# Optimization experiments

Hardware: AMD Instinct MI355X
Metric: run time of the kernel (lower is better)

## Reference

```python
import jax, jax.numpy as jnp
import numpy as np

NUM_HEADS = 32
HEAD_DIM = 128
HEAVY_BUDGET = 256
RECENT_BUDGET = 256
ROPE_BASE = 10000.0


def _rope_tables(position_ids, head_dim, dtype):
    inv_freq = 1.0 / (ROPE_BASE ** (jnp.arange(0, head_dim, 2, dtype=jnp.float32) / head_dim))
    freqs = position_ids.astype(jnp.float32)[..., None] * inv_freq  # [b, s, hd/2]
    emb = jnp.concatenate([freqs, freqs], axis=-1)                  # [b, s, hd]
    return jnp.cos(emb).astype(dtype), jnp.sin(emb).astype(dtype)


def _rotate_half(x):
    h = x.shape[-1] // 2
    return jnp.concatenate([-x[..., h:], x[..., :h]], axis=-1)


def setup_inputs() -> dict:
    key = jax.random.key(0)
    k1, k2, k3, k4, k5 = jax.random.split(key, 5)
    b, s, d = 1, 2048, 4096
    hidden_states = jax.random.normal(k1, (b, s, d), dtype=jnp.float32)
    # additive causal mask, as HF passes into forward
    neg = jnp.finfo(jnp.float32).min
    causal = jnp.tril(jnp.ones((s, s), dtype=bool))
    attention_mask = jnp.where(causal, 0.0, neg).astype(jnp.float32)[None, None]  # [1,1,s,s]
    position_ids = jnp.arange(s, dtype=jnp.int32)[None]  # [1, s]
    scale = 0.02
    Wq = jax.random.normal(k2, (d, d), dtype=jnp.float32) * scale
    Wk = jax.random.normal(k3, (d, d), dtype=jnp.float32) * scale
    Wv = jax.random.normal(k4, (d, d), dtype=jnp.float32) * scale
    Wo = jax.random.normal(k5, (d, d), dtype=jnp.float32) * scale
    return {"hidden_states": hidden_states, "attention_mask": attention_mask,
            "position_ids": position_ids, "Wq": Wq, "Wk": Wk, "Wv": Wv, "Wo": Wo}


def reference(hidden_states, attention_mask, position_ids, Wq, Wk, Wv, Wo):
    b, s, d = hidden_states.shape
    H, hd = NUM_HEADS, HEAD_DIM
    kv = s  # prefill: no past_key_value, masks reset

    # projections: nn.Linear(x) = x @ W.T
    q = (hidden_states @ Wq.T).reshape(b, s, H, hd).transpose(0, 2, 1, 3)  # [b,H,s,hd]
    k = (hidden_states @ Wk.T).reshape(b, s, H, hd).transpose(0, 2, 1, 3)
    v = (hidden_states @ Wv.T).reshape(b, s, H, hd).transpose(0, 2, 1, 3)

    cos, sin = _rope_tables(position_ids, hd, q.dtype)  # [b,s,hd]
    cos, sin = cos[:, None], sin[:, None]               # broadcast over heads
    q = q * cos + _rotate_half(q) * sin
    k = k * cos + _rotate_half(k) * sin

    attn = jnp.einsum('bhqd,bhkd->bhqk', q, k) / np.float32(np.sqrt(hd))
    neg = jnp.finfo(attn.dtype).min
    attn = jnp.maximum(attn + attention_mask, neg)
    # attention_masks_next is None on the first (prefill) call -> no multiplicative mask here
    attn = jax.nn.softmax(attn.astype(jnp.float32), axis=-1).astype(q.dtype)  # [b,H,s,kv]

    # running per-head score accumulation: sum over batch and query dims
    scores = attn.sum(axis=0).sum(axis=1)  # [H, kv]; previous_scores is None at prefill

    # heavy-hitter eviction mask for the next decode step (kv+1 columns)
    mask = jnp.ones((H, kv + 1), dtype=attn.dtype)
    # attn_tokens_all (=kv) > cache_budget, recent_budget > 0:
    mask = mask.at[:, :kv + 1 - RECENT_BUDGET].set(0.0)
    selected = scores[:, :kv - RECENT_BUDGET]                    # drop recent region
    _, keep_topk = jax.lax.top_k(selected, HEAVY_BUDGET)         # [H, heavy]
    mask = mask.at[jnp.arange(H)[:, None], keep_topk].set(1.0)   # scatter heavy hitters
    # torch aliasing: score_mask = attn_mask[:, :-1]; score_mask[:, -recent:] = 1 mutates attn_mask too
    mask = mask.at[:, kv - RECENT_BUDGET:kv].set(1.0)
    attention_masks_next = mask[None, :, None, :]                # [1,H,1,kv+1]
    previous_scores = scores * mask[:, :kv]                      # masked score state

    out = jnp.einsum('bhqk,bhkd->bhqd', attn, v)                 # [b,H,s,hd]
    out = out.transpose(0, 2, 1, 3).reshape(b, s, d) @ Wo.T
    return out, attention_masks_next, previous_scores
```

## Files before the change

kernel.cpp:

```cpp
#include <hip/hip_runtime.h>
#include <hip/hip_bf16.h>
#include <cmath>

#define S_LEN 2048
#define DMODEL 4096
#define NH 32
#define HDIM 128
#define HEAVY 256
#define RECENT 256
#define ATTN_SCALE 0.08838834764831845f
#define NEGBIG -3.0e38f
#define MB (1024ull * 1024ull)

typedef __attribute__((ext_vector_type(8))) short short8v;
typedef __attribute__((ext_vector_type(4))) short short4v;
typedef __attribute__((ext_vector_type(4))) float floatx4;

__device__ inline ushort f2bf(float x) {
  __hip_bfloat16 h = __float2bfloat16(x);
  return __builtin_bit_cast(ushort, h);
}
struct Split3 {
  short a, b, c;
};
__device__ inline Split3 split3(float x) {
  unsigned u = __float_as_uint(x);
  unsigned u1 = u & 0xFFFF0000u;
  float r1 = x - __uint_as_float(u1);
  unsigned u2 = __float_as_uint(r1) & 0xFFFF0000u;
  float r2 = r1 - __uint_as_float(u2);
  unsigned u3 = __float_as_uint(r2);
  Split3 o;
  o.a = (short)(u1 >> 16);
  o.b = (short)(u2 >> 16);
  o.c = (short)(u3 >> 16);
  return o;
}

__device__ __forceinline__ void gl_lds16(const short* gsrc, short* ldst) {
  __builtin_amdgcn_global_load_lds((const __attribute__((address_space(1))) void*)gsrc,
                                   (__attribute__((address_space(3))) void*)ldst, 16, 0, 0);
}

__global__ void split_mat(const float* __restrict__ X, short* __restrict__ Xa,
                          short* __restrict__ Xb, short* __restrict__ Xc, int n4) {
  int stride = gridDim.x * blockDim.x;
  for (int i = blockIdx.x * blockDim.x + threadIdx.x; i < n4; i += stride) {
    float4 v = reinterpret_cast<const float4*>(X)[i];
    float vv[4] = {v.x, v.y, v.z, v.w};
    short4v a, b, c;
#pragma unroll
    for (int j = 0; j < 4; j++) {
      Split3 t = split3(vv[j]);
      a[j] = t.a; b[j] = t.b; c[j] = t.c;
    }
    reinterpret_cast<short4v*>(Xa)[i] = a;
    reinterpret_cast<short4v*>(Xb)[i] = b;
    reinterpret_cast<short4v*>(Xc)[i] = c;
  }
}

__global__ __launch_bounds__(256) void norms_kernel(const float* __restrict__ Qf,
                                                    const float* __restrict__ Kf,
                                                    float* __restrict__ qn,
                                                    float* __restrict__ mk2p) {
  const int h = blockIdx.x >> 4, ch = blockIdx.x & 15;
  const int wv = threadIdx.x >> 6, lane = threadIdx.x & 63;
  __shared__ float wmax[4];
  float mx = 0.f;
  for (int i = 0; i < 32; i++) {
    int r = ch * 128 + wv * 32 + i;
    const float2 qv =
        *reinterpret_cast<const float2*>(&Qf[(size_t)r * DMODEL + h * HDIM + lane * 2]);
    const float2 kv =
        *reinterpret_cast<const float2*>(&Kf[(size_t)r * DMODEL + h * HDIM + lane * 2]);
    float sq = qv.x * qv.x + qv.y * qv.y;
    float sk = kv.x * kv.x + kv.y * kv.y;
#pragma unroll
    for (int off = 1; off <= 32; off <<= 1) {
      sq += __shfl_xor(sq, off);
      sk += __shfl_xor(sk, off);
    }
    if (lane == 0) qn[h * S_LEN + r] = sqrtf(sq);
    mx = fmaxf(mx, sk);
  }
  if (lane == 0) wmax[wv] = mx;
  __syncthreads();
  if (threadIdx.x == 0)
    mk2p[blockIdx.x] = fmaxf(fmaxf(wmax[0], wmax[1]), fmaxf(wmax[2], wmax[3]));
}

__global__ __launch_bounds__(256) void gemm6p(
    const short* __restrict__ Aag, const short* __restrict__ Abg, const short* __restrict__ Acg,
    const short* __restrict__ Bag, const short* __restrict__ Bbg, const short* __restrict__ Bcg,
    float* __restrict__ C, int M, int N, int K) {
  __shared__ short Aa[128 * 40], Ab[128 * 40], Ac[128 * 40];
  __shared__ short Ba[128 * 40], Bb[128 * 40], Bc[128 * 40];
  const int tid = threadIdx.x;
  const int w = tid >> 6, l = tid & 63, g = l >> 4, ln = l & 15;
  const int wm = w >> 1, wn = w & 1;
  const int row0 = blockIdx.y * 128, col0 = blockIdx.x * 128;
  floatx4 acc[4][4] = {};
  for (int k0 = 0; k0 < K; k0 += 32) {
    __syncthreads();
#pragma unroll
    for (int i = 0; i < 2; i++) {
      int id = tid + i * 256;
      int r = id >> 2, c = id & 3;
      size_t ga = (size_t)(row0 + r) * K + k0 + c * 8;
      size_t gb = (size_t)(col0 + r) * K + k0 + c * 8;
      int o = r * 40 + c * 8;
      *reinterpret_cast<short8v*>(&Aa[o]) = *reinterpret_cast<const short8v*>(&Aag[ga]);
      *reinterpret_cast<short8v*>(&Ab[o]) = *reinterpret_cast<const short8v*>(&Abg[ga]);
      *reinterpret_cast<short8v*>(&Ac[o]) = *reinterpret_cast<const short8v*>(&Acg[ga]);
      *reinterpret_cast<short8v*>(&Ba[o]) = *reinterpret_cast<const short8v*>(&Bag[gb]);
      *reinterpret_cast<short8v*>(&Bb[o]) = *reinterpret_cast<const short8v*>(&Bbg[gb]);
      *reinterpret_cast<short8v*>(&Bc[o]) = *reinterpret_cast<const short8v*>(&Bcg[gb]);
    }
    __syncthreads();
#pragma unroll
    for (int i = 0; i < 4; i++) {
      int ar = (wm * 64 + i * 16 + ln) * 40 + g * 8;
      short8v a1 = *reinterpret_cast<const short8v*>(&Aa[ar]);
      short8v a2 = *reinterpret_cast<const short8v*>(&Ab[ar]);
      short8v a3 = *reinterpret_cast<const short8v*>(&Ac[ar]);
#pragma unroll
      for (int j = 0; j < 4; j++) {
        int br = (wn * 64 + j * 16 + ln) * 40 + g * 8;
        short8v b1 = *reinterpret_cast<const short8v*>(&Ba[br]);
        short8v b2 = *reinterpret_cast<const short8v*>(&Bb[br]);
        short8v b3 = *reinterpret_cast<const short8v*>(&Bc[br]);
        acc[i][j] = __builtin_amdgcn_mfma_f32_16x16x32_bf16(a1, b1, acc[i][j], 0, 0, 0);
        acc[i][j] = __builtin_amdgcn_mfma_f32_16x16x32_bf16(a1, b2, acc[i][j], 0, 0, 0);
        acc[i][j] = __builtin_amdgcn_mfma_f32_16x16x32_bf16(a2, b1, acc[i][j], 0, 0, 0);
        acc[i][j] = __builtin_amdgcn_mfma_f32_16x16x32_bf16(a1, b3, acc[i][j], 0, 0, 0);
        acc[i][j] = __builtin_amdgcn_mfma_f32_16x16x32_bf16(a2, b2, acc[i][j], 0, 0, 0);
        acc[i][j] = __builtin_amdgcn_mfma_f32_16x16x32_bf16(a3, b1, acc[i][j], 0, 0, 0);
      }
    }
  }
#pragma unroll
  for (int i = 0; i < 4; i++)
#pragma unroll
    for (int j = 0; j < 4; j++)
#pragma unroll
      for (int r = 0; r < 4; r++)
        C[(size_t)(row0 + wm * 64 + i * 16 + g * 4 + r) * N + col0 + wn * 64 + j * 16 + ln] =
            acc[i][j][r];
}

__global__ __launch_bounds__(256) void gemm6h(const short* __restrict__ Aag,
                                              const short* __restrict__ Abg,
                                              const short* __restrict__ Acg,
                                              const float* __restrict__ B,
                                              float* __restrict__ C, int M, int N, int K) {
  __shared__ short Aa[128 * 40], Ab[128 * 40], Ac[128 * 40];
  __shared__ short Ba[128 * 40], Bb[128 * 40], Bc[128 * 40];
  const int tid = threadIdx.x;
  const int w = tid >> 6, l = tid & 63, g = l >> 4, ln = l & 15;
  const int wm = w >> 1, wn = w & 1;
  const int row0 = blockIdx.y * 128, col0 = blockIdx.x * 128;
  floatx4 acc[4][4] = {};
  for (int k0 = 0; k0 < K; k0 += 32) {
    __syncthreads();
#pragma unroll
    for (int i = 0; i < 2; i++) {
      int id = tid + i * 256;
      int r = id >> 2, c = id & 3;
      size_t ga = (size_t)(row0 + r) * K + k0 + c * 8;
      int o = r * 40 + c * 8;
      *reinterpret_cast<short8v*>(&Aa[o]) = *reinterpret_cast<const short8v*>(&Aag[ga]);
      *reinterpret_cast<short8v*>(&Ab[o]) = *reinterpret_cast<const short8v*>(&Abg[ga]);
      *reinterpret_cast<short8v*>(&Ac[o]) = *reinterpret_cast<const short8v*>(&Acg[ga]);
    }
#pragma unroll
    for (int i = 0; i < 4; i++) {
      int id = tid + i * 256;
      int r = id >> 3, c4 = id & 7;
      float4 bv = *reinterpret_cast<const float4*>(&B[(size_t)(col0 + r) * K + k0 + c4 * 4]);
      float bf[4] = {bv.x, bv.y, bv.z, bv.w};
      short4v b1, b2, b3;
#pragma unroll
      for (int j = 0; j < 4; j++) {
        Split3 t = split3(bf[j]);
        b1[j] = t.a; b2[j] = t.b; b3[j] = t.c;
      }
      int o = r * 40 + c4 * 4;
      *reinterpret_cast<short4v*>(&Ba[o]) = b1;
      *reinterpret_cast<short4v*>(&Bb[o]) = b2;
      *reinterpret_cast<short4v*>(&Bc[o]) = b3;
    }
    __syncthreads();
#pragma unroll
    for (int i = 0; i < 4; i++) {
      int ar = (wm * 64 + i * 16 + ln) * 40 + g * 8;
      short8v a1 = *reinterpret_cast<const short8v*>(&Aa[ar]);
      short8v a2 = *reinterpret_cast<const short8v*>(&Ab[ar]);
      short8v a3 = *reinterpret_cast<const short8v*>(&Ac[ar]);
#pragma unroll
      for (int j = 0; j < 4; j++) {
        int br = (wn * 64 + j * 16 + ln) * 40 + g * 8;
        short8v b1 = *reinterpret_cast<const short8v*>(&Ba[br]);
        short8v b2 = *reinterpret_cast<const short8v*>(&Bb[br]);
        short8v b3 = *reinterpret_cast<const short8v*>(&Bc[br]);
        acc[i][j] = __builtin_amdgcn_mfma_f32_16x16x32_bf16(a1, b1, acc[i][j], 0, 0, 0);
        acc[i][j] = __builtin_amdgcn_mfma_f32_16x16x32_bf16(a1, b2, acc[i][j], 0, 0, 0);
        acc[i][j] = __builtin_amdgcn_mfma_f32_16x16x32_bf16(a2, b1, acc[i][j], 0, 0, 0);
        acc[i][j] = __builtin_amdgcn_mfma_f32_16x16x32_bf16(a1, b3, acc[i][j], 0, 0, 0);
        acc[i][j] = __builtin_amdgcn_mfma_f32_16x16x32_bf16(a2, b2, acc[i][j], 0, 0, 0);
        acc[i][j] = __builtin_amdgcn_mfma_f32_16x16x32_bf16(a3, b1, acc[i][j], 0, 0, 0);
      }
    }
  }
#pragma unroll
  for (int i = 0; i < 4; i++)
#pragma unroll
    for (int j = 0; j < 4; j++)
#pragma unroll
      for (int r = 0; r < 4; r++)
        C[(size_t)(row0 + wm * 64 + i * 16 + g * 4 + r) * N + col0 + wn * 64 + j * 16 + ln] =
            acc[i][j][r];
}

__global__ __launch_bounds__(256) void gemm_bf1(const float* __restrict__ A,
                                                const float* __restrict__ B,
                                                float* __restrict__ C, int M, int N, int K) {
  __shared__ short Ah[128 * 40];
  __shared__ short Bh[128 * 40];
  const int tid = threadIdx.x;
  const int w = tid >> 6, l = tid & 63, g = l >> 4, ln = l & 15;
  const int wm = w >> 1, wn = w & 1;
  const int row0 = blockIdx.y * 128, col0 = blockIdx.x * 128;
  floatx4 acc[4][4] = {};
  for (int k0 = 0; k0 < K; k0 += 32) {
    __syncthreads();
#pragma unroll
    for (int i = 0; i < 4; i++) {
      int id = tid + i * 256;
      int r = id >> 3, c4 = id & 7;
      float4 av = *reinterpret_cast<const float4*>(&A[(size_t)(row0 + r) * K + k0 + c4 * 4]);
      float4 bv = *reinterpret_cast<const float4*>(&B[(size_t)(col0 + r) * K + k0 + c4 * 4]);
      short4v ah, bh;
      ah[0] = (short)f2bf(av.x); ah[1] = (short)f2bf(av.y);
      ah[2] = (short)f2bf(av.z); ah[3] = (short)f2bf(av.w);
      bh[0] = (short)f2bf(bv.x); bh[1] = (short)f2bf(bv.y);
      bh[2] = (short)f2bf(bv.z); bh[3] = (short)f2bf(bv.w);
      *reinterpret_cast<short4v*>(&Ah[r * 40 + c4 * 4]) = ah;
      *reinterpret_cast<short4v*>(&Bh[r * 40 + c4 * 4]) = bh;
    }
    __syncthreads();
#pragma unroll
    for (int i = 0; i < 4; i++) {
      short8v a = *reinterpret_cast<const short8v*>(&Ah[(wm * 64 + i * 16 + ln) * 40 + g * 8]);
#pragma unroll
      for (int j = 0; j < 4; j++) {
        short8v b = *reinterpret_cast<const short8v*>(&Bh[(wn * 64 + j * 16 + ln) * 40 + g * 8]);
        acc[i][j] = __builtin_amdgcn_mfma_f32_16x16x32_bf16(a, b, acc[i][j], 0, 0, 0);
      }
    }
  }
#pragma unroll
  for (int i = 0; i < 4; i++)
#pragma unroll
    for (int j = 0; j < 4; j++)
#pragma unroll
      for (int r = 0; r < 4; r++)
        C[(size_t)(row0 + wm * 64 + i * 16 + g * 4 + r) * N + col0 + wn * 64 + j * 16 + ln] =
            acc[i][j][r];
}

__global__ __launch_bounds__(256) void gemm_vbt(const short* __restrict__ Ab2,
                                                const float* __restrict__ B,
                                                ushort* __restrict__ Vt, int M, int N, int K) {
  __shared__ short Ah[128 * 40];
  __shared__ short Bh[128 * 40];
  const int tid = threadIdx.x;
  const int w = tid >> 6, l = tid & 63, g = l >> 4, ln = l & 15;
  const int wm = w >> 1, wn = w & 1;
  const int row0 = blockIdx.y * 128, col0 = blockIdx.x * 128;
  floatx4 acc[4][4] = {};
  for (int k0 = 0; k0 < K; k0 += 32) {
    __syncthreads();
#pragma unroll
    for (int i = 0; i < 2; i++) {
      int id = tid + i * 256;
      int r = id >> 2, c = id & 3;
      *reinterpret_cast<short8v*>(&Ah[r * 40 + c * 8]) =
          *reinterpret_cast<const short8v*>(&Ab2[(size_t)(row0 + r) * K + k0 + c * 8]);
    }
#pragma unroll
    for (int i = 0; i < 4; i++) {
      int id = tid + i * 256;
      int r = id >> 3, c4 = id & 7;
      float4 bv = *reinterpret_cast<const float4*>(&B[(size_t)(col0 + r) * K + k0 + c4 * 4]);
      short4v bh;
      bh[0] = (short)f2bf(bv.x); bh[1] = (short)f2bf(bv.y);
      bh[2] = (short)f2bf(bv.z); bh[3] = (short)f2bf(bv.w);
      *reinterpret_cast<short4v*>(&Bh[r * 40 + c4 * 4]) = bh;
    }
    __syncthreads();
#pragma unroll
    for (int i = 0; i < 4; i++) {
      short8v a = *reinterpret_cast<const short8v*>(&Ah[(wm * 64 + i * 16 + ln) * 40 + g * 8]);
#pragma unroll
      for (int j = 0; j < 4; j++) {
        short8v b = *reinterpret_cast<const short8v*>(&Bh[(wn * 64 + j * 16 + ln) * 40 + g * 8]);
        acc[i][j] = __builtin_amdgcn_mfma_f32_16x16x32_bf16(a, b, acc[i][j], 0, 0, 0);
      }
    }
  }
#pragma unroll
  for (int i = 0; i < 4; i++)
#pragma unroll
    for (int j = 0; j < 4; j++) {
      short4v o;
#pragma unroll
      for (int r = 0; r < 4; r++) o[r] = (short)f2bf(acc[i][j][r]);
      size_t n = col0 + wn * 64 + j * 16 + ln;
      size_t m0 = row0 + wm * 64 + i * 16 + g * 4;
      *reinterpret_cast<short4v*>(&Vt[n * M + m0]) = o;
    }
}

__global__ void rope_convert(const float* __restrict__ Q, const float* __restrict__ K,
                             const int* __restrict__ pos, short* __restrict__ Qa,
                             short* __restrict__ Qb, short* __restrict__ Qc,
                             short* __restrict__ Ka, short* __restrict__ Kb,
                             short* __restrict__ Kc) {
  int idx = blockIdx.x * blockDim.x + threadIdx.x;
  if (idx >= S_LEN * 64) return;
  int d = idx & 63;
  int r = idx >> 6;
  float p = (float)pos[r];
  float invf = (float)pow(10000.0, -(double)(2 * d) / 128.0);
  float ang = p * invf;
  float c = cosf(ang), s = sinf(ang);
  for (int h = 0; h < NH; h++) {
    size_t base = (size_t)r * DMODEL + h * HDIM + d;
    float q1 = Q[base], q2 = Q[base + 64];
    float k1 = K[base], k2 = K[base + 64];
    float qa = q1 * c - q2 * s, qb = q2 * c + q1 * s;
    float ka = k1 * c - k2 * s, kb = k2 * c + k1 * s;
    Split3 t;
    t = split3(qa); Qa[base] = t.a; Qb[base] = t.b; Qc[base] = t.c;
    t = split3(qb); Qa[base + 64] = t.a; Qb[base + 64] = t.b; Qc[base + 64] = t.c;
    t = split3(ka); Ka[base] = t.a; Kb[base] = t.b; Kc[base] = t.c;
    t = split3(kb); Ka[base + 64] = t.a; Kb[base + 64] = t.b; Kc[base + 64] = t.c;
  }
}

#define KVB 32
#define KSPL (KVB * 128)

__device__ __forceinline__ floatx4 qk6_tile(const short* KaS, const short* KbS,
                                            const short* KcS, const short8v q1[4],
                                            const short8v q2[4], const short8v q3[4],
                                            int krow, int g) {
  floatx4 cA = {}, cB = {}, cC = {}, cD = {}, cE = {}, cF = {};
#pragma unroll
  for (int dc = 0; dc < 4; dc++) {
    int didx = krow * 128 + ((dc * 32 + g * 8) ^ ((krow & 7) << 3));
    short8v k1 = *reinterpret_cast<const short8v*>(&KaS[didx]);
    short8v k2 = *reinterpret_cast<const short8v*>(&KbS[didx]);
    short8v k3 = *reinterpret_cast<const short8v*>(&KcS[didx]);
    cA = __builtin_amdgcn_mfma_f32_16x16x32_bf16(q1[dc], k1, cA, 0, 0, 0);
    cB = __builtin_amdgcn_mfma_f32_16x16x32_bf16(q1[dc], k2, cB, 0, 0, 0);
    cC = __builtin_amdgcn_mfma_f32_16x16x32_bf16(q2[dc], k1, cC, 0, 0, 0);
    cD = __builtin_amdgcn_mfma_f32_16x16x32_bf16(q1[dc], k3, cD, 0, 0, 0);
    cE = __builtin_amdgcn_mfma_f32_16x16x32_bf16(q2[dc], k2, cE, 0, 0, 0);
    cF = __builtin_amdgcn_mfma_f32_16x16x32_bf16(q3[dc], k1, cF, 0, 0, 0);
  }
  return ((cA + cB) + (cC + cD)) + (cE + cF);
}

__device__ __forceinline__ void issue_tile(const short* __restrict__ Ka,
                                           const short* __restrict__ Kb,
                                           const short* __restrict__ Kc, int k0, int h,
                                           short* bufA, short* bufB, short* bufC, int tid) {
  const int wb = tid & 192;
#pragma unroll
  for (int it = 0; it < 2; it++) {
    int j = it * 256 + tid;
    int r = j >> 4, cl = j & 15;
    int cg = cl ^ (r & 7);
    size_t goff = (size_t)(k0 + r) * DMODEL + h * HDIM + cg * 8;
    int cb = (it * 256 + wb) * 8;
    gl_lds16(Ka + goff, bufA + cb);
    gl_lds16(Kb + goff, bufB + cb);
    gl_lds16(Kc + goff, bufC + cb);
  }
}

__global__ __launch_bounds__(256, 3) void attn_fused(
    const short* __restrict__ Qa, const short* __restrict__ Qb, const short* __restrict__ Qc,
    const short* __restrict__ Ka, const short* __restrict__ Kb, const short* __restrict__ Kc,
    const ushort* __restrict__ Vt, const float* __restrict__ qn,
    const float* __restrict__ mk2p, float* __restrict__ AO, float* __restrict__ sp4) {
  __shared__ short KS[2][3][KSPL];
  __shared__ short Ps[4 * 512];
  const int bid = blockIdx.x;
  const int qb = 31 - (bid >> 5);
  const int h = bid & 31;
  const int tid = threadIdx.x;
  const int w = tid >> 6, g = (tid >> 4) & 3, ln = tid & 15;
  const int q0 = qb * 64;
  const int qrow = q0 + w * 16 + ln;
  short8v q1[4], q2[4], q3[4];
#pragma unroll
  for (int dc = 0; dc < 4; dc++) {
    size_t off = (size_t)qrow * DMODEL + h * HDIM + dc * 32 + g * 8;
    q1[dc] = *reinterpret_cast<const short8v*>(&Qa[off]);
    q2[dc] = *reinterpret_cast<const short8v*>(&Qb[off]);
    q3[dc] = *reinterpret_cast<const short8v*>(&Qc[off]);
  }
  float mkv = 0.f;
#pragma unroll
  for (int j = 0; j < 16; j++) mkv = fmaxf(mkv, mk2p[h * 16 + j]);
  const float mk = sqrtf(mkv);
  float B_r[4], l_r[4];
#pragma unroll
  for (int r = 0; r < 4; r++) {
    B_r[r] = qn[h * S_LEN + q0 + w * 16 + g * 4 + r] * mk * ATTN_SCALE;
    l_r[r] = 0.f;
  }
  const int nkt = 2 * qb + 2;

  issue_tile(Ka, Kb, Kc, 0, h, KS[0][0], KS[0][1], KS[0][2], tid);
  __syncthreads();
  for (int t = 0; t < nkt; t++) {
    const int k0 = t * KVB;
    const int cur = t & 1;
    if (t + 1 < nkt)
      issue_tile(Ka, Kb, Kc, k0 + KVB, h, KS[cur ^ 1][0], KS[cur ^ 1][1], KS[cur ^ 1][2], tid);
#pragma unroll
    for (int ct = 0; ct < 2; ct++) {
      floatx4 sacc = qk6_tile(KS[cur][0], KS[cur][1], KS[cur][2], q1, q2, q3, ct * 16 + ln, g);
#pragma unroll
      for (int r = 0; r < 4; r++) {
        float s = sacc[r] * ATTN_SCALE;
        int key = k0 + ct * 16 + ln;
        int qq = q0 + w * 16 + g * 4 + r;
        l_r[r] += (key <= qq) ? __expf(s - B_r[r]) : 0.f;
      }
    }
    __syncthreads();
  }
  float inv_l[4];
#pragma unroll
  for (int r = 0; r < 4; r++) {
    float l = l_r[r];
    l += __shfl_xor(l, 1);
    l += __shfl_xor(l, 2);
    l += __shfl_xor(l, 4);
    l += __shfl_xor(l, 8);
    inv_l[r] = 1.0f / l;
  }

  floatx4 o[8] = {};
  issue_tile(Ka, Kb, Kc, 0, h, KS[0][0], KS[0][1], KS[0][2], tid);
  __syncthreads();
  for (int t = 0; t < nkt; t++) {
    const int k0 = t * KVB;
    const int cur = t & 1;
    if (t + 1 < nkt)
      issue_tile(Ka, Kb, Kc, k0 + KVB, h, KS[cur ^ 1][0], KS[cur ^ 1][1], KS[cur ^ 1][2], tid);
    float pv[2][4];
#pragma unroll
    for (int ct = 0; ct < 2; ct++) {
      floatx4 sacc = qk6_tile(KS[cur][0], KS[cur][1], KS[cur][2], q1, q2, q3, ct * 16 + ln, g);
#pragma unroll
      for (int r = 0; r < 4; r++) {
        float s = sacc[r] * ATTN_SCALE;
        int key = k0 + ct * 16 + ln;
        int qq = q0 + w * 16 + g * 4 + r;
        float e = (key <= qq) ? __expf(s - B_r[r]) : 0.f;
        pv[ct][r] = e * inv_l[r];
      }
    }
#pragma unroll
    for (int ct = 0; ct < 2; ct++) {
      float c2 = pv[ct][0] + pv[ct][1] + pv[ct][2] + pv[ct][3];
      c2 += __shfl_xor(c2, 16);
      c2 += __shfl_xor(c2, 32);
      if (g == 0) sp4[((size_t)(qb * 4 + w) * NH + h) * S_LEN + k0 + ct * 16 + ln] = c2;
    }
#pragma unroll
    for (int ct = 0; ct < 2; ct++)
#pragma unroll
      for (int r = 0; r < 4; r++) {
        int prow = g * 4 + r, pcol = ct * 16 + ln;
        Ps[w * 512 + prow * 32 + (pcol ^ (((prow >> 1) & 1) << 4))] = (short)f2bf(pv[ct][r]);
      }
    short8v pa = *reinterpret_cast<const short8v*>(
        &Ps[w * 512 + ln * 32 + ((g * 8) ^ (((ln >> 1) & 1) << 4))]);
#pragma unroll
    for (int ctd = 0; ctd < 8; ctd++) {
      size_t voff = ((size_t)h * HDIM + ctd * 16 + ln) * S_LEN + k0 + g * 8;
      short8v vb = *reinterpret_cast<const short8v*>(&Vt[voff]);
      o[ctd] = __builtin_amdgcn_mfma_f32_16x16x32_bf16(pa, vb, o[ctd], 0, 0, 0);
    }
    __syncthreads();
  }
#pragma unroll
  for (int ctd = 0; ctd < 8; ctd++)
#pragma unroll
    for (int r = 0; r < 4; r++)
      AO[(size_t)(q0 + w * 16 + g * 4 + r) * DMODEL + h * HDIM + ctd * 16 + ln] = o[ctd][r];
}

__global__ void reduce_scores(const float* __restrict__ sp4, float* __restrict__ scores) {
  int idx = blockIdx.x * blockDim.x + threadIdx.x;
  if (idx >= NH * S_LEN) return;
  int h = idx >> 11, k = idx & 2047;
  float s = 0.f;
  for (int j = 0; j < 128; j++) s += sp4[((size_t)j * NH + h) * S_LEN + k];
  scores[idx] = s;
}

__global__ __launch_bounds__(256) void topk_mask_kernel(const float* __restrict__ scores,
                                                        float* __restrict__ out_mask,
                                                        float* __restrict__ prev_scores) {
  const int h = blockIdx.x;
  __shared__ unsigned sb[S_LEN - RECENT];
  __shared__ int cnt_sh;
  const int NSEL = S_LEN - RECENT;
  const int tid = threadIdx.x;
  const float* sc = scores + (size_t)h * S_LEN;
  for (int i = tid; i < NSEL; i += 256) sb[i] = __float_as_uint(sc[i]);
  __syncthreads();
  unsigned prefix = 0u;
  for (int b = 31; b >= 0; b--) {
    unsigned cand = prefix | (1u << b);
    if (tid == 0) cnt_sh = 0;
    __syncthreads();
    int c = 0;
    for (int i = tid; i < NSEL; i += 256) c += (sb[i] >= cand) ? 1 : 0;
    atomicAdd(&cnt_sh, c);
    __syncthreads();
    if (cnt_sh >= HEAVY) prefix = cand;
    __syncthreads();
  }
  if (tid == 0) cnt_sh = 0;
  __syncthreads();
  int c = 0;
  for (int i = tid; i < NSEL; i += 256) c += (sb[i] > prefix) ? 1 : 0;
  atomicAdd(&cnt_sh, c);
  __syncthreads();
  const int c1 = cnt_sh;
  float* mrow = out_mask + (size_t)h * (S_LEN + 1);
  float* prow = prev_scores + (size_t)h * S_LEN;
  for (int j = NSEL + tid; j < S_LEN + 1; j += 256) mrow[j] = 1.0f;
  for (int k = NSEL + tid; k < S_LEN; k += 256) prow[k] = sc[k];
  for (int i = tid; i < NSEL; i += 256) {
    bool sel = sb[i] > prefix;
    mrow[i] = sel ? 1.f : 0.f;
    prow[i] = sel ? sc[i] : 0.f;
  }
  __syncthreads();
  if (tid == 0) {
    int need = HEAVY - c1;
    for (int i = 0; i < NSEL && need > 0; i++) {
      if (sb[i] == prefix) { mrow[i] = 1.f; prow[i] = sc[i]; need--; }
    }
  }
}

extern "C" void kernel_launch(void* const* d_in, const int* in_sizes, int n_in,
                              void* d_out, int out_size, void* d_ws, size_t ws_size,
                              hipStream_t stream) {
  const float* hidden = (const float*)d_in[0];
  const int* pos = (const int*)d_in[2];
  const float* Wq = (const float*)d_in[3];
  const float* Wk = (const float*)d_in[4];
  const float* Wv = (const float*)d_in[5];
  const float* Wo = (const float*)d_in[6];

  float* out0 = (float*)d_out;
  float* out_mask = out0 + (size_t)S_LEN * DMODEL;
  float* prev_scores = out_mask + (size_t)NH * (S_LEN + 1);

  char* ws = (char*)d_ws;
  float* Qf = (float*)(ws + 0 * MB);
  float* Kf = (float*)(ws + 32 * MB);
  ushort* Vt = (ushort*)(ws + 64 * MB);
  short* Ha = (short*)(ws + 80 * MB);
  short* Hb = (short*)(ws + 96 * MB);
  short* Hc = (short*)(ws + 112 * MB);
  short* Qa = (short*)(ws + 80 * MB);
  short* Qb = (short*)(ws + 96 * MB);
  short* Qc = (short*)(ws + 112 * MB);
  short* Ka = (short*)(ws + 128 * MB);
  short* Kb = (short*)(ws + 144 * MB);
  short* Kc = (short*)(ws + 160 * MB);
  float* AO = Qf;
  float* sp4 = Kf;
  float* scores = (float*)(ws + 64 * MB);

  float* qn = out0;
  float* mk2p = out0 + NH * S_LEN;

  dim3 gg(DMODEL / 128, S_LEN / 128);
  split_mat<<<2048, 256, 0, stream>>>(hidden, Ha, Hb, Hc, S_LEN * DMODEL / 4);

  if (ws_size >= 224 * MB) {
    short* Wsa = (short*)(ws + 128 * MB);
    short* Wsb = (short*)(ws + 160 * MB);
    short* Wsc = (short*)(ws + 192 * MB);
    split_mat<<<2048, 256, 0, stream>>>(Wq, Wsa, Wsb, Wsc, DMODEL * DMODEL / 4);
    gemm6p<<<gg, 256, 0, stream>>>(Ha, Hb, Hc, Wsa, Wsb, Wsc, Qf, S_LEN, DMODEL, DMODEL);
    split_mat<<<2048, 256, 0, stream>>>(Wk, Wsa, Wsb, Wsc, DMODEL * DMODEL / 4);
    gemm6p<<<gg, 256, 0, stream>>>(Ha, Hb, Hc, Wsa, Wsb, Wsc, Kf, S_LEN, DMODEL, DMODEL);
  } else {
    gemm6h<<<gg, 256, 0, stream>>>(Ha, Hb, Hc, Wq, Qf, S_LEN, DMODEL, DMODEL);
    gemm6h<<<gg, 256, 0, stream>>>(Ha, Hb, Hc, Wk, Kf, S_LEN, DMODEL, DMODEL);
  }
  gemm_vbt<<<gg, 256, 0, stream>>>(Ha, Wv, Vt, S_LEN, DMODEL, DMODEL);

  norms_kernel<<<512, 256, 0, stream>>>(Qf, Kf, qn, mk2p);

  int rope_total = S_LEN * 64;
  rope_convert<<<(rope_total + 255) / 256, 256, 0, stream>>>(Qf, Kf, pos, Qa, Qb, Qc, Ka, Kb, Kc);

  hipError_t _e = hipMemsetAsync(sp4, 0, (size_t)128 * NH * S_LEN * sizeof(float), stream);
  (void)_e;
  attn_fused<<<1024, 256, 0, stream>>>(Qa, Qb, Qc, Ka, Kb, Kc, Vt, qn, mk2p, AO, sp4);

  reduce_scores<<<(NH * S_LEN + 255) / 256, 256, 0, stream>>>(sp4, scores);
  topk_mask_kernel<<<NH, 256, 0, stream>>>(scores, out_mask, prev_scores);

  gemm_bf1<<<gg, 256, 0, stream>>>(AO, Wo, out0, S_LEN, DMODEL, DMODEL);
}
```

Before: 1.717 ms.

## Use direct global-to-LDS loads with XOR swizzle in gemm6p; repad other GEMMs

The split-bf16 GEMM now copies tiles straight from global memory into LDS with the gl_lds16 helper, skipping the trip through registers. It uses an unpadded 32-wide layout with an XOR column swizzle to avoid bank conflicts and sets launch_bounds to 3 blocks per SM. The two single-bf16 GEMMs change their LDS row padding from 40 to 56 shorts to change the bank-conflict pattern. The risk is that the swizzle mapping must match the per-wave layout of the direct-to-LDS writes, and that the larger padding raises LDS use.

```diff
diff --git a/kernel.cpp b/kernel.cpp
--- a/kernel.cpp
+++ b/kernel.cpp
@@ -90,46 +90,49 @@
     mk2p[blockIdx.x] = fmaxf(fmaxf(wmax[0], wmax[1]), fmaxf(wmax[2], wmax[3]));
 }
 
-__global__ __launch_bounds__(256) void gemm6p(
+__global__ __launch_bounds__(256, 3) void gemm6p(
     const short* __restrict__ Aag, const short* __restrict__ Abg, const short* __restrict__ Acg,
     const short* __restrict__ Bag, const short* __restrict__ Bbg, const short* __restrict__ Bcg,
     float* __restrict__ C, int M, int N, int K) {
-  __shared__ short Aa[128 * 40], Ab[128 * 40], Ac[128 * 40];
-  __shared__ short Ba[128 * 40], Bb[128 * 40], Bc[128 * 40];
+  __shared__ short LP[6][128 * 32];
   const int tid = threadIdx.x;
   const int w = tid >> 6, l = tid & 63, g = l >> 4, ln = l & 15;
   const int wm = w >> 1, wn = w & 1;
   const int row0 = blockIdx.y * 128, col0 = blockIdx.x * 128;
+  const int wb = tid & 192;
   floatx4 acc[4][4] = {};
   for (int k0 = 0; k0 < K; k0 += 32) {
     __syncthreads();
 #pragma unroll
-    for (int i = 0; i < 2; i++) {
-      int id = tid + i * 256;
-      int r = id >> 2, c = id & 3;
-      size_t ga = (size_t)(row0 + r) * K + k0 + c * 8;
-      size_t gb = (size_t)(col0 + r) * K + k0 + c * 8;
-      int o = r * 40 + c * 8;
-      *reinterpret_cast<short8v*>(&Aa[o]) = *reinterpret_cast<const short8v*>(&Aag[ga]);
-      *reinterpret_cast<short8v*>(&Ab[o]) = *reinterpret_cast<const short8v*>(&Abg[ga]);
-      *reinterpret_cast<short8v*>(&Ac[o]) = *reinterpret_cast<const short8v*>(&Acg[ga]);
-      *reinterpret_cast<short8v*>(&Ba[o]) = *reinterpret_cast<const short8v*>(&Bag[gb]);
-      *reinterpret_cast<short8v*>(&Bb[o]) = *reinterpret_cast<const short8v*>(&Bbg[gb]);
-      *reinterpret_cast<short8v*>(&Bc[o]) = *reinterpret_cast<const short8v*>(&Bcg[gb]);
+    for (int it = 0; it < 2; it++) {
+      int id = it * 256 + tid;
+      int r = id >> 2, j = id & 3;
+      int cg = j ^ ((r >> 1) & 3);
+      size_t ga = (size_t)(row0 + r) * K + k0 + cg * 8;
+      size_t gb = (size_t)(col0 + r) * K + k0 + cg * 8;
+      int cb = (it * 256 + wb) * 8;
+      gl_lds16(Aag + ga, &LP[0][cb]);
+      gl_lds16(Abg + ga, &LP[1][cb]);
+      gl_lds16(Acg + ga, &LP[2][cb]);
+      gl_lds16(Bag + gb, &LP[3][cb]);
+      gl_lds16(Bbg + gb, &LP[4][cb]);
+      gl_lds16(Bcg + gb, &LP[5][cb]);
     }
     __syncthreads();
 #pragma unroll
     for (int i = 0; i < 4; i++) {
-      int ar = (wm * 64 + i * 16 + ln) * 40 + g * 8;
-      short8v a1 = *reinterpret_cast<const short8v*>(&Aa[ar]);
-      short8v a2 = *reinterpret_cast<const short8v*>(&Ab[ar]);
-      short8v a3 = *reinterpret_cast<const short8v*>(&Ac[ar]);
+      int arow = wm * 64 + i * 16 + ln;
+      int aoff = arow * 32 + ((g ^ ((arow >> 1) & 3)) * 8);
+      short8v a1 = *reinterpret_cast<const short8v*>(&LP[0][aoff]);
+      short8v a2 = *reinterpret_cast<const short8v*>(&LP[1][aoff]);
+      short8v a3 = *reinterpret_cast<const short8v*>(&LP[2][aoff]);
 #pragma unroll
       for (int j = 0; j < 4; j++) {
-        int br = (wn * 64 + j * 16 + ln) * 40 + g * 8;
-        short8v b1 = *reinterpret_cast<const short8v*>(&Ba[br]);
-        short8v b2 = *reinterpret_cast<const short8v*>(&Bb[br]);
-        short8v b3 = *reinterpret_cast<const short8v*>(&Bc[br]);
+        int brow = wn * 64 + j * 16 + ln;
+        int boff = brow * 32 + ((g ^ ((brow >> 1) & 3)) * 8);
+        short8v b1 = *reinterpret_cast<const short8v*>(&LP[3][boff]);
+        short8v b2 = *reinterpret_cast<const short8v*>(&LP[4][boff]);
+        short8v b3 = *reinterpret_cast<const short8v*>(&LP[5][boff]);
         acc[i][j] = __builtin_amdgcn_mfma_f32_16x16x32_bf16(a1, b1, acc[i][j], 0, 0, 0);
         acc[i][j] = __builtin_amdgcn_mfma_f32_16x16x32_bf16(a1, b2, acc[i][j], 0, 0, 0);
         acc[i][j] = __builtin_amdgcn_mfma_f32_16x16x32_bf16(a2, b1, acc[i][j], 0, 0, 0);
@@ -225,8 +228,8 @@
 __global__ __launch_bounds__(256) void gemm_bf1(const float* __restrict__ A,
                                                 const float* __restrict__ B,
                                                 float* __restrict__ C, int M, int N, int K) {
-  __shared__ short Ah[128 * 40];
-  __shared__ short Bh[128 * 40];
+  __shared__ short Ah[128 * 56];
+  __shared__ short Bh[128 * 56];
   const int tid = threadIdx.x;
   const int w = tid >> 6, l = tid & 63, g = l >> 4, ln = l & 15;
   const int wm = w >> 1, wn = w & 1;
@@ -245,16 +248,16 @@
       ah[2] = (short)f2bf(av.z); ah[3] = (short)f2bf(av.w);
       bh[0] = (short)f2bf(bv.x); bh[1] = (short)f2bf(bv.y);
       bh[2] = (short)f2bf(bv.z); bh[3] = (short)f2bf(bv.w);
-      *reinterpret_cast<short4v*>(&Ah[r * 40 + c4 * 4]) = ah;
-      *reinterpret_cast<short4v*>(&Bh[r * 40 + c4 * 4]) = bh;
+      *reinterpret_cast<short4v*>(&Ah[r * 56 + c4 * 4]) = ah;
+      *reinterpret_cast<short4v*>(&Bh[r * 56 + c4 * 4]) = bh;
     }
     __syncthreads();
 #pragma unroll
     for (int i = 0; i < 4; i++) {
-      short8v a = *reinterpret_cast<const short8v*>(&Ah[(wm * 64 + i * 16 + ln) * 40 + g * 8]);
+      short8v a = *reinterpret_cast<const short8v*>(&Ah[(wm * 64 + i * 16 + ln) * 56 + g * 8]);
 #pragma unroll
       for (int j = 0; j < 4; j++) {
-        short8v b = *reinterpret_cast<const short8v*>(&Bh[(wn * 64 + j * 16 + ln) * 40 + g * 8]);
+        short8v b = *reinterpret_cast<const short8v*>(&Bh[(wn * 64 + j * 16 + ln) * 56 + g * 8]);
         acc[i][j] = __builtin_amdgcn_mfma_f32_16x16x32_bf16(a, b, acc[i][j], 0, 0, 0);
       }
     }
@@ -272,8 +275,8 @@
 __global__ __launch_bounds__(256) void gemm_vbt(const short* __restrict__ Ab2,
                                                 const float* __restrict__ B,
                                                 ushort* __restrict__ Vt, int M, int N, int K) {
-  __shared__ short Ah[128 * 40];
-  __shared__ short Bh[128 * 40];
+  __shared__ short Ah[128 * 56];
+  __shared__ short Bh[128 * 56];
   const int tid = threadIdx.x;
   const int w = tid >> 6, l = tid & 63, g = l >> 4, ln = l & 15;
   const int wm = w >> 1, wn = w & 1;
@@ -285,7 +288,7 @@
     for (int i = 0; i < 2; i++) {
       int id = tid + i * 256;
       int r = id >> 2, c = id & 3;
-      *reinterpret_cast<short8v*>(&Ah[r * 40 + c * 8]) =
+      *reinterpret_cast<short8v*>(&Ah[r * 56 + c * 8]) =
           *reinterpret_cast<const short8v*>(&Ab2[(size_t)(row0 + r) * K + k0 + c * 8]);
     }
 #pragma unroll
@@ -296,15 +299,15 @@
       short4v bh;
       bh[0] = (short)f2bf(bv.x); bh[1] = (short)f2bf(bv.y);
       bh[2] = (short)f2bf(bv.z); bh[3] = (short)f2bf(bv.w);
-      *reinterpret_cast<short4v*>(&Bh[r * 40 + c4 * 4]) = bh;
+      *reinterpret_cast<short4v*>(&Bh[r * 56 + c4 * 4]) = bh;
     }
     __syncthreads();
 #pragma unroll
     for (int i = 0; i < 4; i++) {
-      short8v a = *reinterpret_cast<const short8v*>(&Ah[(wm * 64 + i * 16 + ln) * 40 + g * 8]);
+      short8v a = *reinterpret_cast<const short8v*>(&Ah[(wm * 64 + i * 16 + ln) * 56 + g * 8]);
 #pragma unroll
       for (int j = 0; j < 4; j++) {
-        short8v b = *reinterpret_cast<const short8v*>(&Bh[(wn * 64 + j * 16 + ln) * 40 + g * 8]);
+        short8v b = *reinterpret_cast<const short8v*>(&Bh[(wn * 64 + j * 16 + ln) * 56 + g * 8]);
         acc[i][j] = __builtin_amdgcn_mfma_f32_16x16x32_bf16(a, b, acc[i][j], 0, 0, 0);
       }
     }
```

New measurement: 1.610 ms. -6.2%, faster.
